# Performance work log

Hardware: AMD Instinct MI355X
Metric: run time of the kernel (lower is better)

## Reference

```python
import jax, jax.numpy as jnp
import numpy as np

_PAULI = {
    'I': np.eye(2, dtype=np.complex64),
    'X': np.array([[0, 1], [1, 0]], dtype=np.complex64),
    'Y': np.array([[0, -1j], [1j, 0]], dtype=np.complex64),
    'Z': np.array([[1, 0], [0, -1]], dtype=np.complex64),
}

OPS = [
    "ZIIIIIIIII", "IZIIIIIIII", "IIZIIIIIII", "IIIZIIIIII",
    "IIIIZIIIII", "IIIIIZIIII", "IIIIIIZIII", "IIIIIIIZII",
    "IIIIIIIIZI", "IIIIIIIIIZ", "XIIIIIIIII", "IXIIIIIIII",
    "IIXIIIIIII", "YIIIIIIIII", "IYIIIIIIII", "IIYIIIIIII",
]

def _op_matrix(s):
    M = _PAULI[s[0]]
    for c in s[1:]:
        M = np.kron(M, _PAULI[c])
    return M

# [n_ops, dim, dim] dense kron-built Pauli observables (dim = 2**10 = 1024)
_OS = np.stack([_op_matrix(s) for s in OPS]).astype(np.complex64)


def setup_inputs() -> dict:
    key = jax.random.key(0)
    x = jax.random.normal(key, (8, 512, 1024), dtype=jnp.float32)
    return {"x": x}


def reference(x):
    B, T, C = x.shape  # (8, 512, 1024)
    dim = _OS.shape[-1]
    # states[:, :C] = x ; here C == dim so pad is a no-op but kept for fidelity
    states = x.reshape(B * T, C).astype(jnp.complex64)
    if C < dim:
        states = jnp.pad(states, ((0, 0), (0, dim - C)))
    Os = jnp.asarray(_OS)  # [O, dim, dim]
    # O_psi[n, o, d] = sum_k Os[o, d, k] * states[n, k]
    opsi = jnp.einsum('odk,nk->nod', Os, states)
    # exp[n, o] = Re( sum_d conj(states[n, d]) * O_psi[n, o, d] )
    exps = jnp.einsum('nd,nod->no', states.conj(), opsi).real
    return exps.reshape(B, T, -1).astype(jnp.float32)
```

## Files before the change

kernel.cpp:

```cpp
#include <hip/hip_runtime.h>

__global__ __launch_bounds__(256) void pauli_exp_half(const float* __restrict__ x,
                                                      float* __restrict__ out) {
    const int wave = threadIdx.x >> 6;
    const int lane = threadIdx.x & 63;
    const int l5   = lane & 31;
    const int row  = blockIdx.x * 8 + wave * 2 + (lane >> 5);

    const float4* rp = reinterpret_cast<const float4*>(x) + (size_t)row * 256;
    float4 v[8];
#pragma unroll
    for (int r = 0; r < 8; ++r) v[r] = rp[r * 32 + l5];

    float t[8], A = 0.f, B = 0.f;
#pragma unroll
    for (int r = 0; r < 8; ++r) {
        const float sx = v[r].x * v[r].x;
        const float sy = v[r].y * v[r].y;
        const float sz = v[r].z * v[r].z;
        const float sw = v[r].w * v[r].w;
        t[r] = (sx + sy) + (sz + sw);
        A += (sx + sy) - (sz + sw);
        B += (sx - sy) + (sz - sw);
    }
    const float t03 = (t[0] + t[1]) + (t[2] + t[3]);
    const float t47 = (t[4] + t[5]) + (t[6] + t[7]);
    const float S   = t03 + t47;
    const float z9  = t03 - t47;
    const float z8  = ((t[0] + t[1]) + (t[4] + t[5])) - ((t[2] + t[3]) + (t[6] + t[7]));
    const float z7  = ((t[0] + t[2]) + (t[4] + t[6])) - ((t[1] + t[3]) + (t[5] + t[7]));

    const float z6 = (l5 & 16) ? -S : S;
    const float z5 = (l5 & 8)  ? -S : S;
    const float z4 = (l5 & 4)  ? -S : S;
    const float z3 = (l5 & 2)  ? -S : S;
    const float z2 = (l5 & 1)  ? -S : S;

    auto dot4 = [](const float4& a, const float4& b) {
        return (a.x * b.x + a.y * b.y) + (a.z * b.z + a.w * b.w);
    };
    const float x512 = 2.f * ((dot4(v[0], v[4]) + dot4(v[1], v[5])) +
                              (dot4(v[2], v[6]) + dot4(v[3], v[7])));
    const float x256 = 2.f * ((dot4(v[0], v[2]) + dot4(v[1], v[3])) +
                              (dot4(v[4], v[6]) + dot4(v[5], v[7])));
    const float x128 = 2.f * ((dot4(v[0], v[1]) + dot4(v[2], v[3])) +
                              (dot4(v[4], v[5]) + dot4(v[6], v[7])));

    float w[16] = {z9, z8, z7, z6, z5, z4, z3, z2, A, B,
                   x512, x256, x128, 0.f, 0.f, 0.f};
    float w8[8];
    {
        const bool hi = lane & 1;
#pragma unroll
        for (int i = 0; i < 8; ++i) {
            const float keep = hi ? w[2 * i + 1] : w[2 * i];
            const float send = hi ? w[2 * i]     : w[2 * i + 1];
            w8[i] = keep + __shfl_xor(send, 1, 64);
        }
    }
    float w4[4];
    {
        const bool hi = lane & 2;
#pragma unroll
        for (int i = 0; i < 4; ++i) {
            const float keep = hi ? w8[2 * i + 1] : w8[2 * i];
            const float send = hi ? w8[2 * i]     : w8[2 * i + 1];
            w4[i] = keep + __shfl_xor(send, 2, 64);
        }
    }
    float w2[2];
    {
        const bool hi = lane & 4;
#pragma unroll
        for (int i = 0; i < 2; ++i) {
            const float keep = hi ? w2[0] * 0.f + (hi ? w4[2 * i + 1] : w4[2 * i]) : w4[2 * i];
            const float k2 = hi ? w4[2 * i + 1] : w4[2 * i];
            const float s2 = hi ? w4[2 * i]     : w4[2 * i + 1];
            w2[i] = k2 + __shfl_xor(s2, 4, 64);
            (void)keep;
        }
    }
    float a;
    {
        const bool hi = lane & 8;
        const float keep = hi ? w2[1] : w2[0];
        const float send = hi ? w2[0] : w2[1];
        a = keep + __shfl_xor(send, 8, 64);
    }
    a += __shfl_xor(a, 16, 64);

    if (l5 < 16) out[(size_t)row * 16 + l5] = a;
}

extern "C" void kernel_launch(void* const* d_in, const int* in_sizes, int n_in,
                              void* d_out, int out_size, void* d_ws, size_t ws_size,
                              hipStream_t stream) {
    const float* x = (const float*)d_in[0];
    float* out = (float*)d_out;
    const int n_rows = in_sizes[0] / 1024;
    pauli_exp_half<<<n_rows / 8, 256, 0, stream>>>(x, out);
}
```

Before: 9.591 us.

## Process each row with 16 lanes instead of 32 to drop a shuffle stage

Each row is now handled by 16 lanes that each load 16 float4 values, instead of 32 lanes loading 8. This removes the final cross-half shuffle, lets every lane write an output, and halves the grid to 256 blocks of 16 rows. The Z-parity sums and the X-pair dot products are rederived for the new index mapping. In exchange each thread holds more registers and there are half as many blocks to hide memory latency, with 16-byte loads strided across lanes.

```diff
diff --git a/kernel.cpp b/kernel.cpp
--- a/kernel.cpp
+++ b/kernel.cpp
@@ -1,20 +1,19 @@
 #include <hip/hip_runtime.h>
 
-__global__ __launch_bounds__(256) void pauli_exp_half(const float* __restrict__ x,
-                                                      float* __restrict__ out) {
-    const int wave = threadIdx.x >> 6;
+__global__ __launch_bounds__(256) void pauli_exp_q(const float* __restrict__ x,
+                                                   float* __restrict__ out) {
     const int lane = threadIdx.x & 63;
-    const int l5   = lane & 31;
-    const int row  = blockIdx.x * 8 + wave * 2 + (lane >> 5);
+    const int l4   = lane & 15;
+    const int row  = blockIdx.x * 16 + ((threadIdx.x >> 6) << 2) + (lane >> 4);
 
     const float4* rp = reinterpret_cast<const float4*>(x) + (size_t)row * 256;
-    float4 v[8];
+    float4 v[16];
 #pragma unroll
-    for (int r = 0; r < 8; ++r) v[r] = rp[r * 32 + l5];
+    for (int r = 0; r < 16; ++r) v[r] = rp[r * 16 + l4];
 
-    float t[8], A = 0.f, B = 0.f;
+    float t[16], A = 0.f, B = 0.f;
 #pragma unroll
-    for (int r = 0; r < 8; ++r) {
+    for (int r = 0; r < 16; ++r) {
         const float sx = v[r].x * v[r].x;
         const float sy = v[r].y * v[r].y;
         const float sz = v[r].z * v[r].z;
@@ -23,30 +22,35 @@
         A += (sx + sy) - (sz + sw);
         B += (sx - sy) + (sz - sw);
     }
-    const float t03 = (t[0] + t[1]) + (t[2] + t[3]);
-    const float t47 = (t[4] + t[5]) + (t[6] + t[7]);
-    const float S   = t03 + t47;
-    const float z9  = t03 - t47;
-    const float z8  = ((t[0] + t[1]) + (t[4] + t[5])) - ((t[2] + t[3]) + (t[6] + t[7]));
-    const float z7  = ((t[0] + t[2]) + (t[4] + t[6])) - ((t[1] + t[3]) + (t[5] + t[7]));
 
-    const float z6 = (l5 & 16) ? -S : S;
-    const float z5 = (l5 & 8)  ? -S : S;
-    const float z4 = (l5 & 4)  ? -S : S;
-    const float z3 = (l5 & 2)  ? -S : S;
-    const float z2 = (l5 & 1)  ? -S : S;
+    float op0 = 0.f, op1 = 0.f, op2 = 0.f, op3 = 0.f, S = 0.f;
+#pragma unroll
+    for (int r = 0; r < 16; ++r) {
+        S += t[r];
+        op0 += (r & 8) ? -t[r] : t[r];
+        op1 += (r & 4) ? -t[r] : t[r];
+        op2 += (r & 2) ? -t[r] : t[r];
+        op3 += (r & 1) ? -t[r] : t[r];
+    }
+
+    const float op4 = (l4 & 8) ? -S : S;
+    const float op5 = (l4 & 4) ? -S : S;
+    const float op6 = (l4 & 2) ? -S : S;
+    const float op7 = (l4 & 1) ? -S : S;
 
     auto dot4 = [](const float4& a, const float4& b) {
         return (a.x * b.x + a.y * b.y) + (a.z * b.z + a.w * b.w);
     };
-    const float x512 = 2.f * ((dot4(v[0], v[4]) + dot4(v[1], v[5])) +
-                              (dot4(v[2], v[6]) + dot4(v[3], v[7])));
-    const float x256 = 2.f * ((dot4(v[0], v[2]) + dot4(v[1], v[3])) +
-                              (dot4(v[4], v[6]) + dot4(v[5], v[7])));
-    const float x128 = 2.f * ((dot4(v[0], v[1]) + dot4(v[2], v[3])) +
-                              (dot4(v[4], v[5]) + dot4(v[6], v[7])));
+    float x512 = 0.f, x256 = 0.f, x128 = 0.f;
+#pragma unroll
+    for (int r = 0; r < 8; ++r) x512 += dot4(v[r], v[r + 8]);
+#pragma unroll
+    for (int r = 0; r < 16; ++r) if (!(r & 4)) x256 += dot4(v[r], v[r | 4]);
+#pragma unroll
+    for (int r = 0; r < 16; ++r) if (!(r & 2)) x128 += dot4(v[r], v[r | 2]);
+    x512 *= 2.f; x256 *= 2.f; x128 *= 2.f;
 
-    float w[16] = {z9, z8, z7, z6, z5, z4, z3, z2, A, B,
+    float w[16] = {op0, op1, op2, op3, op4, op5, op6, op7, A, B,
                    x512, x256, x128, 0.f, 0.f, 0.f};
     float w8[8];
     {
@@ -73,11 +77,9 @@
         const bool hi = lane & 4;
 #pragma unroll
         for (int i = 0; i < 2; ++i) {
-            const float keep = hi ? w2[0] * 0.f + (hi ? w4[2 * i + 1] : w4[2 * i]) : w4[2 * i];
-            const float k2 = hi ? w4[2 * i + 1] : w4[2 * i];
-            const float s2 = hi ? w4[2 * i]     : w4[2 * i + 1];
-            w2[i] = k2 + __shfl_xor(s2, 4, 64);
-            (void)keep;
+            const float keep = hi ? w4[2 * i + 1] : w4[2 * i];
+            const float send = hi ? w4[2 * i]     : w4[2 * i + 1];
+            w2[i] = keep + __shfl_xor(send, 4, 64);
         }
     }
     float a;
@@ -87,9 +89,8 @@
         const float send = hi ? w2[0] : w2[1];
         a = keep + __shfl_xor(send, 8, 64);
     }
-    a += __shfl_xor(a, 16, 64);
 
-    if (l5 < 16) out[(size_t)row * 16 + l5] = a;
+    out[(size_t)row * 16 + l4] = a;
 }
 
 extern "C" void kernel_launch(void* const* d_in, const int* in_sizes, int n_in,
@@ -98,5 +99,5 @@
     const float* x = (const float*)d_in[0];
     float* out = (float*)d_out;
     const int n_rows = in_sizes[0] / 1024;
-    pauli_exp_half<<<n_rows / 8, 256, 0, stream>>>(x, out);
+    pauli_exp_q<<<n_rows / 16, 256, 0, stream>>>(x, out);
 }
```

After: 17.53 us. 1.83x slower.
